# Kernel optimization log

Measured on AMD Instinct MI355X. Metric: run time of the kernel, lower is better.

Reference implementation:

```python
import jax, jax.numpy as jnp
import numpy as np

B, T, C, HD = 4, 2048, 1024, 64

def setup_inputs() -> dict:
    key = jax.random.key(0)
    kx, kq, kk, kv = jax.random.split(key, 4)
    # Weights stored as [n_embed, head_size]; equivalent to torch Linear weight transposed.
    scale = 1.0 / np.sqrt(C)
    return {
        "x": jax.random.normal(kx, (B, T, C), dtype=jnp.float32),
        "Wq": jax.random.normal(kq, (C, HD), dtype=jnp.float32) * scale,
        "Wk": jax.random.normal(kk, (C, HD), dtype=jnp.float32) * scale,
        "Wv": jax.random.normal(kv, (C, HD), dtype=jnp.float32) * scale,
    }

def reference(x, Wq, Wk, Wv):
    # Projections (no bias)
    q = x @ Wq  # [B,T,HD]
    k = x @ Wk
    v = x @ Wv
    hd = k.shape[-1]
    # NOTE: original multiplies by sqrt(head_size) (not the usual 1/sqrt) -- faithful.
    scores = jnp.einsum("btd,bsd->bts", q, k) * (hd ** 0.5)  # [B,T,T]
    # First softmax over full (unmasked) rows
    w = jax.nn.softmax(scores, axis=-1)
    # Causal mask applied AFTER the first softmax, then a second softmax
    causal = jnp.tril(jnp.ones((q.shape[1], q.shape[1]), dtype=bool))  # [T,T]
    w = jnp.where(causal[None, :, :], w, -jnp.inf)
    w = jax.nn.softmax(w, axis=-1)
    out = jnp.einsum("bts,bsd->btd", w, v)  # [B,T,HD]
    return out
```

## Files before the change

### kernel.cpp

```cpp
#include <hip/hip_runtime.h>
#include <math.h>

#define T_  2048
#define C_  1024
#define HD_ 64

typedef __attribute__((ext_vector_type(8))) short bf16x8;
typedef __attribute__((ext_vector_type(4))) float f32x4;

#define MFMA_BF16(A, B, C) __builtin_amdgcn_mfma_f32_16x16x32_bf16(A, B, C, 0, 0, 0)

#define QSCALE 11.54156032711171f

#define EXP2F(x) __builtin_amdgcn_exp2f(x)

__device__ __forceinline__ short f2bf(float f) {
    union { float f; unsigned u; } v; v.f = f;
    unsigned r = v.u + 0x7fffu + ((v.u >> 16) & 1u);
    return (short)(r >> 16);
}
__device__ __forceinline__ float bf2f(short s) {
    union { float f; unsigned u; } v;
    v.u = ((unsigned)(unsigned short)s) << 16;
    return v.f;
}

__global__ __launch_bounds__(256) void prep_w_kernel(
    const float* __restrict__ Wq, const float* __restrict__ Wk,
    const float* __restrict__ Wv, short* __restrict__ wtf)
{
    const int m = blockIdx.y;
    const float* W = (m == 0) ? Wq : (m == 1) ? Wk : Wv;
    const int t = threadIdx.x;
    const int c = blockIdx.x * 64 + (t >> 2);
    const int hg = (t & 3) * 16;
    const int ct = m * 4 + (t & 3);
    const int c0i = c >> 6, kc = (c >> 5) & 1, lq = (c >> 3) & 3, e = c & 7;
    const float4* wp = (const float4*)(W + (size_t)c * HD_ + hg);
    #pragma unroll
    for (int u = 0; u < 4; ++u) {
        float4 f = wp[u];
        float vs[4] = {f.x, f.y, f.z, f.w};
        #pragma unroll
        for (int ei = 0; ei < 4; ++ei) {
            int h16 = u * 4 + ei;
            int L = h16 + 16 * lq;
            short hh = f2bf(vs[ei]);
            short lo = f2bf(vs[ei] - bf2f(hh));
            size_t oh = ((((size_t)(ct * 2 + 0) * 16 + c0i) * 2 + kc) * 64 + L) * 8 + e;
            size_t ol = ((((size_t)(ct * 2 + 1) * 16 + c0i) * 2 + kc) * 64 + L) * 8 + e;
            wtf[oh] = hh;
            wtf[ol] = lo;
        }
    }
}

__global__ __launch_bounds__(256) void qkv_proj_kernel(
    const float* __restrict__ x, const short* __restrict__ wtf,
    short* __restrict__ qhp, short* __restrict__ qlp,
    short* __restrict__ khp, short* __restrict__ klp,
    short* __restrict__ vtp)
{
    __shared__ __align__(16) short xh[2][16 * 64], xl[2][16 * 64];

    const int t = threadIdx.x, L = t & 63, wv = t >> 6;
    const int R0 = blockIdx.x * 16;
    const int ctq = wv;

    f32x4 acc[3];
    #pragma unroll
    for (int j = 0; j < 3; ++j) acc[j] = {0.f, 0.f, 0.f, 0.f};

    const int xrow = t >> 4, xc4 = t & 15;
    const float* xp = x + (size_t)(R0 + xrow) * C_ + xc4 * 4;
    float4 xa;
    auto loadX = [&](int c0) { xa = *(const float4*)(xp + c0); };

    const int c8 = xc4 >> 1, xhalf = xc4 & 1;
    const int slot = xrow * 64 + ((c8 ^ (xrow & 7)) * 8) + xhalf * 4;
    auto stageX = [&](int buf) {
        float vs[4] = {xa.x, xa.y, xa.z, xa.w};
        short4 vh, vl;
        short* vhp = (short*)&vh; short* vlp = (short*)&vl;
        #pragma unroll
        for (int e = 0; e < 4; ++e) {
            short hh = f2bf(vs[e]);
            vhp[e] = hh;
            vlp[e] = f2bf(vs[e] - bf2f(hh));
        }
        *(short4*)&xh[buf][slot] = vh;
        *(short4*)&xl[buf][slot] = vl;
    };

    const size_t lo8 = (size_t)L * 8;
    auto loadWF = [&](int c0i, int kc, bf16x8* w) {
        w[0] = *(const bf16x8*)(wtf + (size_t)((((ctq + 0) * 2 + 0) * 16 + c0i) * 2 + kc) * 512 + lo8);
        w[1] = *(const bf16x8*)(wtf + (size_t)((((ctq + 0) * 2 + 1) * 16 + c0i) * 2 + kc) * 512 + lo8);
        w[2] = *(const bf16x8*)(wtf + (size_t)((((ctq + 4) * 2 + 0) * 16 + c0i) * 2 + kc) * 512 + lo8);
        w[3] = *(const bf16x8*)(wtf + (size_t)((((ctq + 4) * 2 + 1) * 16 + c0i) * 2 + kc) * 512 + lo8);
        w[4] = *(const bf16x8*)(wtf + (size_t)((((ctq + 8) * 2 + 0) * 16 + c0i) * 2 + kc) * 512 + lo8);
    };

    bf16x8 wf0[5], wf1[5];
    const int arow = L & 15;

    loadX(0);
    loadWF(0, 0, wf0);
    stageX(0);
    loadX(64);
    __syncthreads();

    for (int c0i = 0; c0i < 16; ++c0i) {
        const int cur = c0i & 1;
        if (c0i < 15) {
            stageX(cur ^ 1);
            if (c0i < 14) loadX((c0i + 2) * 64);
        }
        loadWF(c0i, 1, wf1);
        {
            int ch = (L >> 4);
            int off = arow * 64 + ((ch ^ (arow & 7)) * 8);
            bf16x8 axh = *(const bf16x8*)&xh[cur][off];
            bf16x8 axl = *(const bf16x8*)&xl[cur][off];
            acc[0] = MFMA_BF16(axl, wf0[0], acc[0]);
            acc[0] = MFMA_BF16(axh, wf0[1], acc[0]);
            acc[0] = MFMA_BF16(axh, wf0[0], acc[0]);
            acc[1] = MFMA_BF16(axl, wf0[2], acc[1]);
            acc[1] = MFMA_BF16(axh, wf0[3], acc[1]);
            acc[1] = MFMA_BF16(axh, wf0[2], acc[1]);
            acc[2] = MFMA_BF16(wf0[4], axh, acc[2]);
        }
        if (c0i < 15) loadWF(c0i + 1, 0, wf0);
        {
            int ch = 4 + (L >> 4);
            int off = arow * 64 + ((ch ^ (arow & 7)) * 8);
            bf16x8 axh = *(const bf16x8*)&xh[cur][off];
            bf16x8 axl = *(const bf16x8*)&xl[cur][off];
            acc[0] = MFMA_BF16(axl, wf1[0], acc[0]);
            acc[0] = MFMA_BF16(axh, wf1[1], acc[0]);
            acc[0] = MFMA_BF16(axh, wf1[0], acc[0]);
            acc[1] = MFMA_BF16(axl, wf1[2], acc[1]);
            acc[1] = MFMA_BF16(axh, wf1[3], acc[1]);
            acc[1] = MFMA_BF16(axh, wf1[2], acc[1]);
            acc[2] = MFMA_BF16(wf1[4], axh, acc[2]);
        }
        __syncthreads();
    }

    const int quad = L >> 4;
    #pragma unroll
    for (int r = 0; r < 4; ++r) {
        int row = R0 + quad * 4 + r;
        int h = ctq * 16 + (L & 15);
        float vq = acc[0][r] * QSCALE;
        short hq = f2bf(vq);
        qhp[(size_t)row * HD_ + h] = hq;
        qlp[(size_t)row * HD_ + h] = f2bf(vq - bf2f(hq));
        float vk = acc[1][r];
        short hk = f2bf(vk);
        khp[(size_t)row * HD_ + h] = hk;
        klp[(size_t)row * HD_ + h] = f2bf(vk - bf2f(hk));
        int d = ctq * 16 + quad * 4 + r;
        int tt = R0 + (L & 15);
        int bb = tt >> 11, tl = tt & (T_ - 1);
        vtp[(size_t)(bb * 64 + d) * T_ + tl] = f2bf(acc[2][r]);
    }
}

__global__ __launch_bounds__(512) void fused_attn_kernel(
    const short* __restrict__ qhp, const short* __restrict__ qlp,
    const short* __restrict__ khp, const short* __restrict__ klp,
    const short* __restrict__ vtp, float* __restrict__ sc,
    float* __restrict__ out)
{
    __shared__ float red[8][16][2];
    __shared__ float msl[16];
    __shared__ float ored[8][16][64];
    __shared__ float dred[8][16];

    const int t = threadIdx.x, L = t & 63, wv = t >> 6;
    const int k = blockIdx.x >> 1, half = blockIdx.x & 1;
    const int b = k >> 6, j = k & 63;
    const int p = half ? (127 - j) : j;
    const int T0 = p * 16;

    {
        const int cho = (L >> 4) * 8;
        bf16x8 qfh[2], qfl[2];
        #pragma unroll
        for (int dc = 0; dc < 2; ++dc) {
            int row = T0 + (L & 15);
            size_t off = ((size_t)b * T_ + row) * HD_ + dc * 32 + cho;
            qfh[dc] = *(const bf16x8*)(qhp + off);
            qfl[dc] = *(const bf16x8*)(qlp + off);
        }

        const int colbase = wv * 256 + (L & 15);
        const short* kbh = khp + ((size_t)b * T_ + colbase) * HD_ + cho;
        const short* kbl = klp + ((size_t)b * T_ + colbase) * HD_ + cho;

        bf16x8 kfh[2][2], kfl[2][2];
        auto loadK = [&](int ct, bf16x8 kh[2], bf16x8 kl[2]) {
            #pragma unroll
            for (int dc = 0; dc < 2; ++dc) {
                kh[dc] = *(const bf16x8*)(kbh + (size_t)ct * 16 * HD_ + dc * 32);
                kl[dc] = *(const bf16x8*)(kbl + (size_t)ct * 16 * HD_ + dc * 32);
            }
        };
        loadK(0, kfh[0], kfl[0]);

        float ml[4], ll[4];
        #pragma unroll
        for (int r = 0; r < 4; ++r) { ml[r] = -1e30f; ll[r] = 0.f; }

        #pragma unroll
        for (int bq = 0; bq < 4; ++bq) {
            f32x4 sv[4];
            #pragma unroll
            for (int jj = 0; jj < 4; ++jj) {
                const int ct = bq * 4 + jj;
                const int cb = ct & 1;
                if (ct < 15) loadK(ct + 1, kfh[cb ^ 1], kfl[cb ^ 1]);
                f32x4 s = {0.f, 0.f, 0.f, 0.f};
                #pragma unroll
                for (int dc = 0; dc < 2; ++dc) {
                    s = MFMA_BF16(qfl[dc], kfh[cb][dc], s);
                    s = MFMA_BF16(qfh[dc], kfl[cb][dc], s);
                    s = MFMA_BF16(qfh[dc], kfh[cb][dc], s);
                }
                sv[jj] = s;
                if (wv * 256 + ct * 16 <= T0 + 15) {
                    #pragma unroll
                    for (int r = 0; r < 4; ++r) {
                        int row = T0 + (L >> 4) * 4 + r;
                        sc[((size_t)b * T_ + row) * T_ + colbase + ct * 16] = s[r];
                    }
                }
            }
            #pragma unroll
            for (int r = 0; r < 4; ++r) {
                float v0 = sv[0][r], v1 = sv[1][r], v2 = sv[2][r], v3 = sv[3][r];
                float mb = fmaxf(fmaxf(v0, v1), fmaxf(v2, v3));
                float lb = EXP2F(v0 - mb) + EXP2F(v1 - mb)
                         + EXP2F(v2 - mb) + EXP2F(v3 - mb);
                float mn = fmaxf(ml[r], mb);
                ll[r] = ll[r] * EXP2F(ml[r] - mn) + lb * EXP2F(mb - mn);
                ml[r] = mn;
            }
        }
        #pragma unroll
        for (int off = 1; off < 16; off <<= 1)
            #pragma unroll
            for (int r = 0; r < 4; ++r) {
                float mo = __shfl_xor(ml[r], off, 64);
                float lo = __shfl_xor(ll[r], off, 64);
                float mn = fmaxf(ml[r], mo);
                ll[r] = ll[r] * EXP2F(ml[r] - mn) + lo * EXP2F(mo - mn);
                ml[r] = mn;
            }
        if ((L & 15) == 0) {
            #pragma unroll
            for (int r = 0; r < 4; ++r) {
                red[wv][(L >> 4) * 4 + r][0] = ml[r];
                red[wv][(L >> 4) * 4 + r][1] = ll[r];
            }
        }
    }
    __syncthreads();
    if (t < 16) {
        float M = red[0][t][0], S = red[0][t][1];
        #pragma unroll
        for (int w = 1; w < 8; ++w) {
            float mo = red[w][t][0], lo = red[w][t][1];
            float mn = fmaxf(M, mo);
            S = S * EXP2F(M - mn) + lo * EXP2F(mo - mn);
            M = mn;
        }
        msl[t] = M + __log2f(S);
    }
    __syncthreads();

    const int row = T0 + (L & 15);
    const float mls = msl[L & 15];
    const float* srow = sc + ((size_t)b * T_ + row) * T_;
    const short* vb = vtp + (size_t)b * 64 * T_;
    const int nJ = (T0 + 271) >> 8;
    const int cq = (L >> 4) * 8;

    f32x4 ov[4];
    #pragma unroll
    for (int dt = 0; dt < 4; ++dt) ov[dt] = {0.f, 0.f, 0.f, 0.f};
    float dn = 0.f;

    float4 sa0, sa1, sb0, sb1;
    bf16x8 va0, va1, va2, va3, vb0, vb1, vb2, vb3;

#define LDS_(jt, s0, s1) { int c0_ = (jt) * 256 + wv * 32 + cq;                  \
        s0 = *(const float4*)(srow + c0_); s1 = *(const float4*)(srow + c0_ + 4); }
#define LDV_(jt, v0, v1, v2, v3) { int c0_ = (jt) * 256 + wv * 32 + cq;          \
        v0 = *(const bf16x8*)(vb + (size_t)( 0 + (L & 15)) * T_ + c0_);          \
        v1 = *(const bf16x8*)(vb + (size_t)(16 + (L & 15)) * T_ + c0_);          \
        v2 = *(const bf16x8*)(vb + (size_t)(32 + (L & 15)) * T_ + c0_);          \
        v3 = *(const bf16x8*)(vb + (size_t)(48 + (L & 15)) * T_ + c0_); }
#define BODY_(jt, s0, s1, v0, v1, v2, v3) {                                      \
        const int c0_ = (jt) * 256 + wv * 32 + cq;                               \
        float vs_[8] = {s0.x, s0.y, s0.z, s0.w, s1.x, s1.y, s1.z, s1.w};         \
        bf16x8 ef_;                                                              \
        _Pragma("unroll")                                                        \
        for (int e = 0; e < 8; ++e) {                                            \
            float pvv = EXP2F(vs_[e] - mls);                                     \
            float evv = (c0_ + e <= row) ? __expf(pvv) : 0.f;                    \
            dn += evv;                                                           \
            ef_[e] = f2bf(evv);                                                  \
        }                                                                        \
        ov[0] = MFMA_BF16(ef_, v0, ov[0]);                                       \
        ov[1] = MFMA_BF16(ef_, v1, ov[1]);                                       \
        ov[2] = MFMA_BF16(ef_, v2, ov[2]);                                       \
        ov[3] = MFMA_BF16(ef_, v3, ov[3]); }

    LDS_(0, sa0, sa1)
    LDV_(0, va0, va1, va2, va3)
    int jt = 0;
    for (; jt + 2 <= nJ; jt += 2) {
        LDS_(jt + 1, sb0, sb1)
        LDV_(jt + 1, vb0, vb1, vb2, vb3)
        BODY_(jt, sa0, sa1, va0, va1, va2, va3)
        if (jt + 2 < nJ) {
            LDS_(jt + 2, sa0, sa1)
            LDV_(jt + 2, va0, va1, va2, va3)
        }
        BODY_(jt + 1, sb0, sb1, vb0, vb1, vb2, vb3)
    }
    if (jt < nJ) {
        BODY_(jt, sa0, sa1, va0, va1, va2, va3)
    }
#undef LDS_
#undef LDV_
#undef BODY_

    dn += __shfl_xor(dn, 16, 64);
    dn += __shfl_xor(dn, 32, 64);
    if (L < 16) dred[wv][L] = dn;
    #pragma unroll
    for (int dt = 0; dt < 4; ++dt)
        #pragma unroll
        for (int r = 0; r < 4; ++r)
            ored[wv][(L >> 4) * 4 + r][dt * 16 + (L & 15)] = ov[dt][r];
    __syncthreads();

    const int orow = t >> 5, d0 = (t & 31) * 2;
    float D = 0.f;
    #pragma unroll
    for (int w = 0; w < 8; ++w) D += dred[w][orow];
    float di = 1.f / D;
    float o0 = 0.f, o1 = 0.f;
    #pragma unroll
    for (int w = 0; w < 8; ++w) {
        o0 += ored[w][orow][d0 + 0];
        o1 += ored[w][orow][d0 + 1];
    }
    float2 o = make_float2(o0 * di, o1 * di);
    *(float2*)(out + ((size_t)b * T_ + T0 + orow) * HD_ + d0) = o;
}

extern "C" void kernel_launch(void* const* d_in, const int* in_sizes, int n_in,
                              void* d_out, int out_size, void* d_ws, size_t ws_size,
                              hipStream_t stream) {
    (void)in_sizes; (void)n_in; (void)out_size; (void)ws_size;
    const float* x  = (const float*)d_in[0];
    const float* Wq = (const float*)d_in[1];
    const float* Wk = (const float*)d_in[2];
    const float* Wv = (const float*)d_in[3];
    float* outp = (float*)d_out;

    char* ws = (char*)d_ws;
    short* wt  = (short*)ws;
    short* qh = (short*)(ws + 786432);
    short* ql = (short*)(ws + 786432 + 1048576);
    short* kh = (short*)(ws + 786432 + 2 * 1048576);
    short* kl = (short*)(ws + 786432 + 3 * 1048576);
    short* vt = (short*)(ws + 786432 + 4 * 1048576);
    float* sc = (float*)(ws + 8388608);

    prep_w_kernel<<<dim3(16, 3), 256, 0, stream>>>(Wq, Wk, Wv, wt);
    qkv_proj_kernel<<<dim3(512), 256, 0, stream>>>(x, wt, qh, ql, kh, kl, vt);
    fused_attn_kernel<<<dim3(512), 512, 0, stream>>>(qh, ql, kh, kl, vt, sc, outp);
}
```

Before: 147.5 us.

## Recompute causal QK scores in second pass instead of spilling scores to global memory

The attention kernel previously wrote the causal part of the fp32 score matrix to a global workspace during the first (row-max/sum) pass and read it back for the second softmax and PV product. Now the second pass recomputes the QK^T tiles with the split-bf16 MFMAs, exponentiates them, and stages the probabilities through an XOR-swizzled shared-memory buffer. Each wave then owns one 16-wide slice of the head dimension and one half of the 256-column chunk. This removes a large global write/read of scores, but it roughly doubles QK MFMA work and adds two block barriers per 256-column chunk.

Measured after the change: 167.4 us. +13.5%, slower.

```diff
diff --git a/kernel.cpp b/kernel.cpp
--- a/kernel.cpp
+++ b/kernel.cpp
@@ -170,32 +170,32 @@
 __global__ __launch_bounds__(512) void fused_attn_kernel(
     const short* __restrict__ qhp, const short* __restrict__ qlp,
     const short* __restrict__ khp, const short* __restrict__ klp,
-    const short* __restrict__ vtp, float* __restrict__ sc,
-    float* __restrict__ out)
+    const short* __restrict__ vtp, float* __restrict__ out)
 {
     __shared__ float red[8][16][2];
     __shared__ float msl[16];
-    __shared__ float ored[8][16][64];
-    __shared__ float dred[8][16];
+    __shared__ __align__(16) float es[16][2][128];
+    __shared__ float ored2[8][16][16];
+    __shared__ float dred[2][16];
 
     const int t = threadIdx.x, L = t & 63, wv = t >> 6;
     const int k = blockIdx.x >> 1, half = blockIdx.x & 1;
     const int b = k >> 6, j = k & 63;
     const int p = half ? (127 - j) : j;
     const int T0 = p * 16;
+    const int q4 = L >> 4, m16 = L & 15;
+    const int cho = q4 * 8;
+
+    bf16x8 qfh[2], qfl[2];
+    #pragma unroll
+    for (int dc = 0; dc < 2; ++dc) {
+        size_t off = ((size_t)b * T_ + T0 + m16) * HD_ + dc * 32 + cho;
+        qfh[dc] = *(const bf16x8*)(qhp + off);
+        qfl[dc] = *(const bf16x8*)(qlp + off);
+    }
 
     {
-        const int cho = (L >> 4) * 8;
-        bf16x8 qfh[2], qfl[2];
-        #pragma unroll
-        for (int dc = 0; dc < 2; ++dc) {
-            int row = T0 + (L & 15);
-            size_t off = ((size_t)b * T_ + row) * HD_ + dc * 32 + cho;
-            qfh[dc] = *(const bf16x8*)(qhp + off);
-            qfl[dc] = *(const bf16x8*)(qlp + off);
-        }
-
-        const int colbase = wv * 256 + (L & 15);
+        const int colbase = wv * 256 + m16;
         const short* kbh = khp + ((size_t)b * T_ + colbase) * HD_ + cho;
         const short* kbl = klp + ((size_t)b * T_ + colbase) * HD_ + cho;
 
@@ -229,13 +229,6 @@
                     s = MFMA_BF16(qfh[dc], kfh[cb][dc], s);
                 }
                 sv[jj] = s;
-                if (wv * 256 + ct * 16 <= T0 + 15) {
-                    #pragma unroll
-                    for (int r = 0; r < 4; ++r) {
-                        int row = T0 + (L >> 4) * 4 + r;
-                        sc[((size_t)b * T_ + row) * T_ + colbase + ct * 16] = s[r];
-                    }
-                }
             }
             #pragma unroll
             for (int r = 0; r < 4; ++r) {
@@ -258,11 +251,11 @@
                 ll[r] = ll[r] * EXP2F(ml[r] - mn) + lo * EXP2F(mo - mn);
                 ml[r] = mn;
             }
-        if ((L & 15) == 0) {
+        if (m16 == 0) {
             #pragma unroll
             for (int r = 0; r < 4; ++r) {
-                red[wv][(L >> 4) * 4 + r][0] = ml[r];
-                red[wv][(L >> 4) * 4 + r][1] = ll[r];
+                red[wv][q4 * 4 + r][0] = ml[r];
+                red[wv][q4 * 4 + r][1] = ll[r];
             }
         }
     }
@@ -280,85 +273,109 @@
     }
     __syncthreads();
 
-    const int row = T0 + (L & 15);
-    const float mls = msl[L & 15];
-    const float* srow = sc + ((size_t)b * T_ + row) * T_;
-    const short* vb = vtp + (size_t)b * 64 * T_;
-    const int nJ = (T0 + 271) >> 8;
-    const int cq = (L >> 4) * 8;
-
-    f32x4 ov[4];
-    #pragma unroll
-    for (int dt = 0; dt < 4; ++dt) ov[dt] = {0.f, 0.f, 0.f, 0.f};
+    const int CE = T0 + 16;
+    const int nC = (CE + 255) >> 8;
+    const int dt = wv & 3, chal = wv >> 2;
+
+    f32x4 ov = {0.f, 0.f, 0.f, 0.f};
     float dn = 0.f;
-
-    float4 sa0, sa1, sb0, sb1;
-    bf16x8 va0, va1, va2, va3, vb0, vb1, vb2, vb3;
-
-#define LDS_(jt, s0, s1) { int c0_ = (jt) * 256 + wv * 32 + cq;                  \
-        s0 = *(const float4*)(srow + c0_); s1 = *(const float4*)(srow + c0_ + 4); }
-#define LDV_(jt, v0, v1, v2, v3) { int c0_ = (jt) * 256 + wv * 32 + cq;          \
-        v0 = *(const bf16x8*)(vb + (size_t)( 0 + (L & 15)) * T_ + c0_);          \
-        v1 = *(const bf16x8*)(vb + (size_t)(16 + (L & 15)) * T_ + c0_);          \
-        v2 = *(const bf16x8*)(vb + (size_t)(32 + (L & 15)) * T_ + c0_);          \
-        v3 = *(const bf16x8*)(vb + (size_t)(48 + (L & 15)) * T_ + c0_); }
-#define BODY_(jt, s0, s1, v0, v1, v2, v3) {                                      \
-        const int c0_ = (jt) * 256 + wv * 32 + cq;                               \
-        float vs_[8] = {s0.x, s0.y, s0.z, s0.w, s1.x, s1.y, s1.z, s1.w};         \
-        bf16x8 ef_;                                                              \
-        _Pragma("unroll")                                                        \
-        for (int e = 0; e < 8; ++e) {                                            \
-            float pvv = EXP2F(vs_[e] - mls);                                     \
-            float evv = (c0_ + e <= row) ? __expf(pvv) : 0.f;                    \
-            dn += evv;                                                           \
-            ef_[e] = f2bf(evv);                                                  \
-        }                                                                        \
-        ov[0] = MFMA_BF16(ef_, v0, ov[0]);                                       \
-        ov[1] = MFMA_BF16(ef_, v1, ov[1]);                                       \
-        ov[2] = MFMA_BF16(ef_, v2, ov[2]);                                       \
-        ov[3] = MFMA_BF16(ef_, v3, ov[3]); }
-
-    LDS_(0, sa0, sa1)
-    LDV_(0, va0, va1, va2, va3)
-    int jt = 0;
-    for (; jt + 2 <= nJ; jt += 2) {
-        LDS_(jt + 1, sb0, sb1)
-        LDV_(jt + 1, vb0, vb1, vb2, vb3)
-        BODY_(jt, sa0, sa1, va0, va1, va2, va3)
-        if (jt + 2 < nJ) {
-            LDS_(jt + 2, sa0, sa1)
-            LDV_(jt + 2, va0, va1, va2, va3)
-        }
-        BODY_(jt + 1, sb0, sb1, vb0, vb1, vb2, vb3)
-    }
-    if (jt < nJ) {
-        BODY_(jt, sa0, sa1, va0, va1, va2, va3)
-    }
-#undef LDS_
-#undef LDV_
-#undef BODY_
+    const short* vrow = vtp + (size_t)b * 64 * T_ + (size_t)(dt * 16 + m16) * T_;
+
+    for (int cc = 0; cc < nC; ++cc) {
+        {
+            const int ct0 = cc * 16 + wv;
+            const int ct1 = ct0 + 8;
+            const bool a0 = ct0 * 16 < CE, a1 = ct1 * 16 < CE;
+            bf16x8 k0h[2], k0l[2], k1h[2], k1l[2];
+            if (a0) {
+                const short* ph = khp + ((size_t)b * T_ + ct0 * 16 + m16) * HD_ + cho;
+                const short* pl = klp + ((size_t)b * T_ + ct0 * 16 + m16) * HD_ + cho;
+                k0h[0] = *(const bf16x8*)ph;        k0h[1] = *(const bf16x8*)(ph + 32);
+                k0l[0] = *(const bf16x8*)pl;        k0l[1] = *(const bf16x8*)(pl + 32);
+            }
+            if (a1) {
+                const short* ph = khp + ((size_t)b * T_ + ct1 * 16 + m16) * HD_ + cho;
+                const short* pl = klp + ((size_t)b * T_ + ct1 * 16 + m16) * HD_ + cho;
+                k1h[0] = *(const bf16x8*)ph;        k1h[1] = *(const bf16x8*)(ph + 32);
+                k1l[0] = *(const bf16x8*)pl;        k1l[1] = *(const bf16x8*)(pl + 32);
+            }
+            float e0[4] = {0.f, 0.f, 0.f, 0.f}, e1[4] = {0.f, 0.f, 0.f, 0.f};
+            if (a0) {
+                f32x4 s = {0.f, 0.f, 0.f, 0.f};
+                #pragma unroll
+                for (int dc = 0; dc < 2; ++dc) {
+                    s = MFMA_BF16(qfl[dc], k0h[dc], s);
+                    s = MFMA_BF16(qfh[dc], k0l[dc], s);
+                    s = MFMA_BF16(qfh[dc], k0h[dc], s);
+                }
+                #pragma unroll
+                for (int r = 0; r < 4; ++r) {
+                    int colg = ct0 * 16 + m16, rowg = T0 + q4 * 4 + r;
+                    float pvv = EXP2F(s[r] - msl[q4 * 4 + r]);
+                    e0[r] = (colg <= rowg) ? __expf(pvv) : 0.f;
+                }
+            }
+            if (a1) {
+                f32x4 s = {0.f, 0.f, 0.f, 0.f};
+                #pragma unroll
+                for (int dc = 0; dc < 2; ++dc) {
+                    s = MFMA_BF16(qfl[dc], k1h[dc], s);
+                    s = MFMA_BF16(qfh[dc], k1l[dc], s);
+                    s = MFMA_BF16(qfh[dc], k1h[dc], s);
+                }
+                #pragma unroll
+                for (int r = 0; r < 4; ++r) {
+                    int colg = ct1 * 16 + m16, rowg = T0 + q4 * 4 + r;
+                    float pvv = EXP2F(s[r] - msl[q4 * 4 + r]);
+                    e1[r] = (colg <= rowg) ? __expf(pvv) : 0.f;
+                }
+            }
+            const int cl = wv * 16 + m16;
+            #pragma unroll
+            for (int r = 0; r < 4; ++r) {
+                int rw = q4 * 4 + r;
+                int idx = (((cl >> 3) ^ rw) & 15) * 8 + (cl & 7);
+                es[rw][0][idx] = e0[r];
+                es[rw][1][idx] = e1[r];
+            }
+        }
+        __syncthreads();
+        {
+            const int cbase = cc * 256 + chal * 128;
+            #pragma unroll
+            for (int sub = 0; sub < 4; ++sub) {
+                int chunk = ((sub * 4 + q4) ^ m16) & 15;
+                const float* ep = &es[m16][chal][chunk * 8];
+                float4 x0 = *(const float4*)ep;
+                float4 x1 = *(const float4*)(ep + 4);
+                float ev[8] = {x0.x, x0.y, x0.z, x0.w, x1.x, x1.y, x1.z, x1.w};
+                bf16x8 pf;
+                #pragma unroll
+                for (int e = 0; e < 8; ++e) {
+                    dn += ev[e];
+                    pf[e] = f2bf(ev[e]);
+                }
+                bf16x8 vf = *(const bf16x8*)(vrow + cbase + sub * 32 + q4 * 8);
+                ov = MFMA_BF16(pf, vf, ov);
+            }
+        }
+        __syncthreads();
+    }
 
     dn += __shfl_xor(dn, 16, 64);
     dn += __shfl_xor(dn, 32, 64);
-    if (L < 16) dred[wv][L] = dn;
+    if (dt == 0 && L < 16) dred[chal][L] = dn;
     #pragma unroll
-    for (int dt = 0; dt < 4; ++dt)
-        #pragma unroll
-        for (int r = 0; r < 4; ++r)
-            ored[wv][(L >> 4) * 4 + r][dt * 16 + (L & 15)] = ov[dt][r];
+    for (int r = 0; r < 4; ++r)
+        ored2[wv][q4 * 4 + r][m16] = ov[r];
     __syncthreads();
 
     const int orow = t >> 5, d0 = (t & 31) * 2;
-    float D = 0.f;
-    #pragma unroll
-    for (int w = 0; w < 8; ++w) D += dred[w][orow];
+    float D = dred[0][orow] + dred[1][orow];
     float di = 1.f / D;
-    float o0 = 0.f, o1 = 0.f;
-    #pragma unroll
-    for (int w = 0; w < 8; ++w) {
-        o0 += ored[w][orow][d0 + 0];
-        o1 += ored[w][orow][d0 + 1];
-    }
+    const int dti = d0 >> 4;
+    float o0 = ored2[dti][orow][d0 & 15]       + ored2[dti + 4][orow][d0 & 15];
+    float o1 = ored2[dti][orow][(d0 + 1) & 15] + ored2[dti + 4][orow][(d0 + 1) & 15];
     float2 o = make_float2(o0 * di, o1 * di);
     *(float2*)(out + ((size_t)b * T_ + T0 + orow) * HD_ + d0) = o;
 }
@@ -380,9 +397,8 @@
     short* kh = (short*)(ws + 786432 + 2 * 1048576);
     short* kl = (short*)(ws + 786432 + 3 * 1048576);
     short* vt = (short*)(ws + 786432 + 4 * 1048576);
-    float* sc = (float*)(ws + 8388608);
 
     prep_w_kernel<<<dim3(16, 3), 256, 0, stream>>>(Wq, Wk, Wv, wt);
     qkv_proj_kernel<<<dim3(512), 256, 0, stream>>>(x, wt, qh, ql, kh, kl, vt);
-    fused_attn_kernel<<<dim3(512), 512, 0, stream>>>(qh, ql, kh, kl, vt, sc, outp);
-}
+    fused_attn_kernel<<<dim3(512), 512, 0, stream>>>(qh, ql, kh, kl, vt, outp);
+}
```
